# Kernel tuning notes

Hardware: AMD Instinct MI355X
Metric: run time of the kernel (lower is better)

The kernel has to match this reference:

```python
import jax, jax.numpy as jnp
import numpy as np

N = 25000      # number of target nodes
K = 32         # sampled neighbor fanout
F_IN = 256
F_OUT = 256


def setup_inputs() -> dict:
    key = jax.random.key(0)
    k1, k2, k3, k4 = jax.random.split(key, 4)
    x = jax.random.normal(k1, (N, F_IN), dtype=jnp.float32)
    neigh = jax.random.randint(k2, (N, K), 0, N, dtype=jnp.int64)
    # Linear(in_feats, out_feats) parameters
    W = jax.random.normal(k3, (F_IN, F_OUT), dtype=jnp.float32) / np.sqrt(F_IN)
    b = jax.random.normal(k4, (F_OUT,), dtype=jnp.float32) * 0.01
    return {"x": x, "neigh": neigh, "W": W, "b": b}


def reference(x, neigh, W, b):
    # Gather neighbor features: [N, K, F_IN]
    h = x[neigh]
    # Linear + ReLU transform on each neighbor feature
    h = jax.nn.relu(jnp.einsum('nkf,fo->nko', h, W) + b)
    # Element-wise max-pool across the neighbor set -> [N, F_OUT]
    return jnp.max(h, axis=1)
```

## Files before the change

### kernel.cpp

```cpp
#include <hip/hip_runtime.h>
#include <hip/hip_bf16.h>

#define N_NODES 25000
#define KFAN    32
#define FIN     256
#define FOUT    256

typedef float  f32x4  __attribute__((ext_vector_type(4)));
typedef short  s16x8  __attribute__((ext_vector_type(8)));

__device__ __forceinline__ ushort f2bf(float f) {
    unsigned int u = __float_as_uint(f);
    u += 0x7fffu + ((u >> 16) & 1u);
    return (ushort)(u >> 16);
}
__device__ __forceinline__ unsigned int pack2(float a, float b) {
    return (unsigned int)f2bf(a) | ((unsigned int)f2bf(b) << 16);
}

__global__ __launch_bounds__(256) void transpose_w(
    const float* __restrict__ W, ushort* __restrict__ Wt)
{
    __shared__ float ls[32][33];
    const int bid = blockIdx.x;
    const int kt  = bid & 7;
    const int nt  = bid >> 3;
    const int t   = threadIdx.x;

    {
        int kl = t >> 3, n4 = (t & 7) * 4;
        float4 v = *(const float4*)(W + (size_t)(kt * 32 + kl) * FOUT + nt * 32 + n4);
        ls[kl][n4 + 0] = v.x; ls[kl][n4 + 1] = v.y;
        ls[kl][n4 + 2] = v.z; ls[kl][n4 + 3] = v.w;
    }
    __syncthreads();
    {
        int nl = t >> 3, k4 = (t & 7) * 4;
        ushort4 o;
        o.x = f2bf(ls[k4 + 0][nl]);
        o.y = f2bf(ls[k4 + 1][nl]);
        o.z = f2bf(ls[k4 + 2][nl]);
        o.w = f2bf(ls[k4 + 3][nl]);
        *(ushort4*)(Wt + (size_t)(nt * 32 + nl) * FIN + kt * 32 + k4) = o;
    }
}

__global__ __launch_bounds__(256) void gemm_mfma(
    const float*  __restrict__ x,
    const ushort* __restrict__ Wt,
    const float*  __restrict__ bias,
    ushort*       __restrict__ y)
{
    __shared__ ushort As[64][72];

    const int tid  = threadIdx.x;
    const int lane = tid & 63;
    const int wv   = tid >> 6;
    const int l16  = lane & 15;
    const int q    = lane >> 4;
    const int row0 = blockIdx.x * 64;
    const int n0   = blockIdx.y * 128 + wv * 32;

    f32x4 acc[4][2];
    #pragma unroll
    for (int i = 0; i < 4; ++i)
        #pragma unroll
        for (int j = 0; j < 2; ++j) acc[i][j] = (f32x4)0.f;

    const int r    = tid >> 2;
    const int kcol = (tid & 3) * 16;

    for (int kc = 0; kc < FIN; kc += 64) {
        float4 v0 = make_float4(0.f,0.f,0.f,0.f), v1 = v0, v2 = v0, v3 = v0;
        int gr = row0 + r;
        if (gr < N_NODES) {
            const float* p = x + (size_t)gr * FIN + kc + kcol;
            v0 = *(const float4*)p;
            v1 = *(const float4*)(p + 4);
            v2 = *(const float4*)(p + 8);
            v3 = *(const float4*)(p + 12);
        }
        uint4 pa, pb;
        pa.x = pack2(v0.x, v0.y); pa.y = pack2(v0.z, v0.w);
        pa.z = pack2(v1.x, v1.y); pa.w = pack2(v1.z, v1.w);
        pb.x = pack2(v2.x, v2.y); pb.y = pack2(v2.z, v2.w);
        pb.z = pack2(v3.x, v3.y); pb.w = pack2(v3.z, v3.w);
        *(uint4*)&As[r][kcol]     = pa;
        *(uint4*)&As[r][kcol + 8] = pb;
        __syncthreads();

        #pragma unroll
        for (int kk = 0; kk < 64; kk += 32) {
            const int k0 = kk + q * 8;
            s16x8 a[4], b[2];
            #pragma unroll
            for (int mt = 0; mt < 4; ++mt)
                a[mt] = *(const s16x8*)&As[mt * 16 + l16][k0];
            #pragma unroll
            for (int ct = 0; ct < 2; ++ct)
                b[ct] = *(const s16x8*)(Wt + (size_t)(n0 + ct * 16 + l16) * FIN + kc + k0);
            #pragma unroll
            for (int mt = 0; mt < 4; ++mt)
                #pragma unroll
                for (int ct = 0; ct < 2; ++ct)
                    acc[mt][ct] = __builtin_amdgcn_mfma_f32_16x16x32_bf16(a[mt], b[ct], acc[mt][ct], 0, 0, 0);
        }
        __syncthreads();
    }

    #pragma unroll
    for (int ct = 0; ct < 2; ++ct) {
        const int col = n0 + ct * 16 + l16;
        const float bv = bias[col];
        #pragma unroll
        for (int mt = 0; mt < 4; ++mt) {
            #pragma unroll
            for (int rr = 0; rr < 4; ++rr) {
                int row = row0 + mt * 16 + q * 4 + rr;
                if (row < N_NODES)
                    y[(size_t)row * FOUT + col] = f2bf(fmaxf(acc[mt][ct][rr] + bv, 0.f));
            }
        }
    }
}

__global__ __launch_bounds__(256) void pool_max(
    const ushort* __restrict__ y,
    const int*    __restrict__ neigh,
    float*        __restrict__ out)
{
    const int bid   = blockIdx.x;
    const int chunk = bid & 3;
    const int nb    = bid >> 2;
    const int tid   = threadIdx.x;
    const int lane  = tid & 63;
    const int g     = lane >> 3;
    const int gl    = lane & 7;
    const int wv    = tid >> 6;

    const int n  = nb * 32 + wv * 8 + g;
    const int nc = n < N_NODES ? n : N_NODES - 1;

    const int4 iv = *(const int4*)(neigh + (size_t)nc * KFAN + gl * 4);
    const int base8 = lane & 56;
    int ia[4] = {iv.x, iv.y, iv.z, iv.w};

    const ushort* yc = y + chunk * 64 + gl * 8;

    s16x8 acc = (s16x8)0;
    #pragma unroll
    for (int k = 0; k < KFAN; ++k) {
        int idx = __shfl(ia[k & 3], base8 + (k >> 2));
        s16x8 cur = *(const s16x8*)(yc + (size_t)idx * FOUT);
        acc = __builtin_elementwise_max(acc, cur);
    }

    if (n < N_NODES) {
        f32x4 o0, o1;
        o0.x = __uint_as_float(((unsigned int)(ushort)acc[0]) << 16);
        o0.y = __uint_as_float(((unsigned int)(ushort)acc[1]) << 16);
        o0.z = __uint_as_float(((unsigned int)(ushort)acc[2]) << 16);
        o0.w = __uint_as_float(((unsigned int)(ushort)acc[3]) << 16);
        o1.x = __uint_as_float(((unsigned int)(ushort)acc[4]) << 16);
        o1.y = __uint_as_float(((unsigned int)(ushort)acc[5]) << 16);
        o1.z = __uint_as_float(((unsigned int)(ushort)acc[6]) << 16);
        o1.w = __uint_as_float(((unsigned int)(ushort)acc[7]) << 16);
        float* op = out + (size_t)n * FOUT + chunk * 64 + gl * 8;
        __builtin_nontemporal_store(o0, (f32x4*)op);
        __builtin_nontemporal_store(o1, (f32x4*)(op + 4));
    }
}

extern "C" void kernel_launch(void* const* d_in, const int* in_sizes, int n_in,
                              void* d_out, int out_size, void* d_ws, size_t ws_size,
                              hipStream_t stream) {
    const float* x     = (const float*)d_in[0];
    const int*   neigh = (const int*)  d_in[1];
    const float* W     = (const float*)d_in[2];
    const float* bias  = (const float*)d_in[3];
    float*       out   = (float*)d_out;
    ushort*      y     = (ushort*)d_ws;
    ushort*      Wt    = (ushort*)d_out;

    transpose_w<<<64, 256, 0, stream>>>(W, Wt);

    dim3 g1((N_NODES + 63) / 64, 2);
    gemm_mfma<<<g1, 256, 0, stream>>>(x, Wt, bias, y);

    const int nblocks = ((N_NODES + 31) / 32) * 4;
    pool_max<<<nblocks, 256, 0, stream>>>(y, neigh, out);
}
```

Before: 118.6 us.

## Load full-K A tile once, swizzle GEMM blocks, stage pool indices in LDS

The GEMM now loads the whole 64x256 row tile of x into LDS up front, dropping the per-K-chunk syncs, and remaps a 1D grid so both column halves of the same rows run close together for L2 reuse. It also uses the hardware packed bf16 convert instruction and sets occupancy launch bounds. The pool kernel stages neighbor indices in LDS instead of using shuffles and splits the max into two accumulators to expose more independent loads. The larger LDS tile and the 16 float4 register loads per thread may limit occupancy.

```diff
diff --git a/kernel.cpp b/kernel.cpp
--- a/kernel.cpp
+++ b/kernel.cpp
@@ -14,8 +14,11 @@
     u += 0x7fffu + ((u >> 16) & 1u);
     return (ushort)(u >> 16);
 }
+
 __device__ __forceinline__ unsigned int pack2(float a, float b) {
-    return (unsigned int)f2bf(a) | ((unsigned int)f2bf(b) << 16);
+    unsigned int r;
+    asm("v_cvt_pk_bf16_f32 %0, %1, %2" : "=v"(r) : "v"(a), "v"(b));
+    return r;
 }
 
 __global__ __launch_bounds__(256) void transpose_w(
@@ -45,21 +48,47 @@
     }
 }
 
-__global__ __launch_bounds__(256) void gemm_mfma(
+__global__ __launch_bounds__(256, 4) void gemm_mfma(
     const float*  __restrict__ x,
     const ushort* __restrict__ Wt,
     const float*  __restrict__ bias,
     ushort*       __restrict__ y)
 {
-    __shared__ ushort As[64][72];
+    __shared__ ushort As[64][264];
 
     const int tid  = threadIdx.x;
     const int lane = tid & 63;
     const int wv   = tid >> 6;
     const int l16  = lane & 15;
     const int q    = lane >> 4;
-    const int row0 = blockIdx.x * 64;
-    const int n0   = blockIdx.y * 128 + wv * 32;
+
+    const int b = blockIdx.x;
+    int rb, cb;
+    if (b < 768) { rb = ((b >> 4) << 3) + (b & 7); cb = (b >> 3) & 1; }
+    else         { const int t2 = b - 768; rb = 384 + (t2 >> 1); cb = t2 & 1; }
+    const int row0 = rb * 64;
+    const int n0   = cb * 128 + wv * 32;
+
+    {
+        const int r     = tid >> 2;
+        const int kbase = (tid & 3) * 64;
+        int gr = row0 + r;
+        if (gr >= N_NODES) gr = N_NODES - 1;
+        const float* p = x + (size_t)gr * FIN + kbase;
+        float4 v[16];
+        #pragma unroll
+        for (int i = 0; i < 16; ++i) v[i] = *(const float4*)(p + i * 4);
+        #pragma unroll
+        for (int i = 0; i < 8; ++i) {
+            uint4 pk;
+            pk.x = pack2(v[2*i].x,     v[2*i].y);
+            pk.y = pack2(v[2*i].z,     v[2*i].w);
+            pk.z = pack2(v[2*i+1].x,   v[2*i+1].y);
+            pk.w = pack2(v[2*i+1].z,   v[2*i+1].w);
+            *(uint4*)&As[r][kbase + i * 8] = pk;
+        }
+    }
+    __syncthreads();
 
     f32x4 acc[4][2];
     #pragma unroll
@@ -67,45 +96,23 @@
         #pragma unroll
         for (int j = 0; j < 2; ++j) acc[i][j] = (f32x4)0.f;
 
-    const int r    = tid >> 2;
-    const int kcol = (tid & 3) * 16;
-
-    for (int kc = 0; kc < FIN; kc += 64) {
-        float4 v0 = make_float4(0.f,0.f,0.f,0.f), v1 = v0, v2 = v0, v3 = v0;
-        int gr = row0 + r;
-        if (gr < N_NODES) {
-            const float* p = x + (size_t)gr * FIN + kc + kcol;
-            v0 = *(const float4*)p;
-            v1 = *(const float4*)(p + 4);
-            v2 = *(const float4*)(p + 8);
-            v3 = *(const float4*)(p + 12);
-        }
-        uint4 pa, pb;
-        pa.x = pack2(v0.x, v0.y); pa.y = pack2(v0.z, v0.w);
-        pa.z = pack2(v1.x, v1.y); pa.w = pack2(v1.z, v1.w);
-        pb.x = pack2(v2.x, v2.y); pb.y = pack2(v2.z, v2.w);
-        pb.z = pack2(v3.x, v3.y); pb.w = pack2(v3.z, v3.w);
-        *(uint4*)&As[r][kcol]     = pa;
-        *(uint4*)&As[r][kcol + 8] = pb;
-        __syncthreads();
-
-        #pragma unroll
-        for (int kk = 0; kk < 64; kk += 32) {
-            const int k0 = kk + q * 8;
-            s16x8 a[4], b[2];
-            #pragma unroll
-            for (int mt = 0; mt < 4; ++mt)
-                a[mt] = *(const s16x8*)&As[mt * 16 + l16][k0];
+    const ushort* wp0 = Wt + (size_t)(n0 + l16) * FIN;
+    const ushort* wp1 = wp0 + (size_t)16 * FIN;
+
+    #pragma unroll
+    for (int kk = 0; kk < FIN; kk += 32) {
+        const int k0 = kk + q * 8;
+        s16x8 a[4], bfr[2];
+        bfr[0] = *(const s16x8*)(wp0 + k0);
+        bfr[1] = *(const s16x8*)(wp1 + k0);
+        #pragma unroll
+        for (int mt = 0; mt < 4; ++mt)
+            a[mt] = *(const s16x8*)&As[mt * 16 + l16][k0];
+        #pragma unroll
+        for (int mt = 0; mt < 4; ++mt)
             #pragma unroll
             for (int ct = 0; ct < 2; ++ct)
-                b[ct] = *(const s16x8*)(Wt + (size_t)(n0 + ct * 16 + l16) * FIN + kc + k0);
-            #pragma unroll
-            for (int mt = 0; mt < 4; ++mt)
-                #pragma unroll
-                for (int ct = 0; ct < 2; ++ct)
-                    acc[mt][ct] = __builtin_amdgcn_mfma_f32_16x16x32_bf16(a[mt], b[ct], acc[mt][ct], 0, 0, 0);
-        }
-        __syncthreads();
+                acc[mt][ct] = __builtin_amdgcn_mfma_f32_16x16x32_bf16(a[mt], bfr[ct], acc[mt][ct], 0, 0, 0);
     }
 
     #pragma unroll
@@ -129,42 +136,55 @@
     const int*    __restrict__ neigh,
     float*        __restrict__ out)
 {
+    __shared__ int nidx[32][36];
+
     const int bid   = blockIdx.x;
     const int chunk = bid & 3;
     const int nb    = bid >> 2;
     const int tid   = threadIdx.x;
-    const int lane  = tid & 63;
-    const int g     = lane >> 3;
-    const int gl    = lane & 7;
-    const int wv    = tid >> 6;
-
-    const int n  = nb * 32 + wv * 8 + g;
-    const int nc = n < N_NODES ? n : N_NODES - 1;
-
-    const int4 iv = *(const int4*)(neigh + (size_t)nc * KFAN + gl * 4);
-    const int base8 = lane & 56;
-    int ia[4] = {iv.x, iv.y, iv.z, iv.w};
+
+    {
+        const int nl = tid >> 3, k4 = (tid & 7) * 4;
+        int gn = nb * 32 + nl;
+        if (gn >= N_NODES) gn = N_NODES - 1;
+        *(int4*)&nidx[nl][k4] = *(const int4*)(neigh + (size_t)gn * KFAN + k4);
+    }
+    __syncthreads();
+
+    const int lane   = tid & 63;
+    const int g      = lane >> 3;
+    const int gl     = lane & 7;
+    const int wv     = tid >> 6;
+    const int node_l = wv * 8 + g;
+    const int n      = nb * 32 + node_l;
 
     const ushort* yc = y + chunk * 64 + gl * 8;
 
-    s16x8 acc = (s16x8)0;
-    #pragma unroll
-    for (int k = 0; k < KFAN; ++k) {
-        int idx = __shfl(ia[k & 3], base8 + (k >> 2));
-        s16x8 cur = *(const s16x8*)(yc + (size_t)idx * FOUT);
-        acc = __builtin_elementwise_max(acc, cur);
-    }
+    s16x8 acc0 = (s16x8)0, acc1 = (s16x8)0;
+    #pragma unroll
+    for (int k = 0; k < KFAN; k += 4) {
+        const int4 ii = *(const int4*)&nidx[node_l][k];
+        s16x8 c0 = *(const s16x8*)(yc + (size_t)ii.x * FOUT);
+        s16x8 c1 = *(const s16x8*)(yc + (size_t)ii.y * FOUT);
+        s16x8 c2 = *(const s16x8*)(yc + (size_t)ii.z * FOUT);
+        s16x8 c3 = *(const s16x8*)(yc + (size_t)ii.w * FOUT);
+        acc0 = __builtin_elementwise_max(acc0, c0);
+        acc1 = __builtin_elementwise_max(acc1, c1);
+        acc0 = __builtin_elementwise_max(acc0, c2);
+        acc1 = __builtin_elementwise_max(acc1, c3);
+    }
+    acc0 = __builtin_elementwise_max(acc0, acc1);
 
     if (n < N_NODES) {
         f32x4 o0, o1;
-        o0.x = __uint_as_float(((unsigned int)(ushort)acc[0]) << 16);
-        o0.y = __uint_as_float(((unsigned int)(ushort)acc[1]) << 16);
-        o0.z = __uint_as_float(((unsigned int)(ushort)acc[2]) << 16);
-        o0.w = __uint_as_float(((unsigned int)(ushort)acc[3]) << 16);
-        o1.x = __uint_as_float(((unsigned int)(ushort)acc[4]) << 16);
-        o1.y = __uint_as_float(((unsigned int)(ushort)acc[5]) << 16);
-        o1.z = __uint_as_float(((unsigned int)(ushort)acc[6]) << 16);
-        o1.w = __uint_as_float(((unsigned int)(ushort)acc[7]) << 16);
+        o0.x = __uint_as_float(((unsigned int)(ushort)acc0[0]) << 16);
+        o0.y = __uint_as_float(((unsigned int)(ushort)acc0[1]) << 16);
+        o0.z = __uint_as_float(((unsigned int)(ushort)acc0[2]) << 16);
+        o0.w = __uint_as_float(((unsigned int)(ushort)acc0[3]) << 16);
+        o1.x = __uint_as_float(((unsigned int)(ushort)acc0[4]) << 16);
+        o1.y = __uint_as_float(((unsigned int)(ushort)acc0[5]) << 16);
+        o1.z = __uint_as_float(((unsigned int)(ushort)acc0[6]) << 16);
+        o1.w = __uint_as_float(((unsigned int)(ushort)acc0[7]) << 16);
         float* op = out + (size_t)n * FOUT + chunk * 64 + gl * 8;
         __builtin_nontemporal_store(o0, (f32x4*)op);
         __builtin_nontemporal_store(o1, (f32x4*)(op + 4));
@@ -184,8 +204,7 @@
 
     transpose_w<<<64, 256, 0, stream>>>(W, Wt);
 
-    dim3 g1((N_NODES + 63) / 64, 2);
-    gemm_mfma<<<g1, 256, 0, stream>>>(x, Wt, bias, y);
+    gemm_mfma<<<782, 256, 0, stream>>>(x, Wt, bias, y);
 
     const int nblocks = ((N_NODES + 31) / 32) * 4;
     pool_max<<<nblocks, 256, 0, stream>>>(y, neigh, out);
```

Result: no change. 120.9 us (+1.9%).
